# Kernel optimization log

Hardware: AMD Instinct MI355X
Metric: run time of the kernel (lower is better)

The kernel has to match this reference:

```python
import jax, jax.numpy as jnp
import numpy as np

LTH_THOLD = 0.0

def _mlp(x, w1, b1, w2, b2, w3, b3):
    # x: [b,h,s,d]; w*: [h,in,out]; per-head 3-layer MLP with SiLU
    h1 = jax.nn.silu(jnp.einsum('bhsd,hde->bhse', x, w1) + b1[None, :, None, :])
    h2 = jax.nn.silu(jnp.einsum('bhsd,hde->bhse', h1, w2) + b2[None, :, None, :])
    return jnp.einsum('bhsd,hde->bhse', h2, w3) + b3[None, :, None, :]

def setup_inputs() -> dict:
    key = jax.random.key(0)
    ks = jax.random.split(key, 16)
    b, h, s, d, idim, fdim = 2, 32, 2048, 128, 128, 32
    sc1 = 1.0 / np.sqrt(d); sc2 = 1.0 / np.sqrt(idim)
    def lin(k, fan_in, shape, sc):
        return jax.random.uniform(k, shape, jnp.float32, -sc, sc)
    inp = {
        'K': jax.random.normal(ks[0], (b, h, s, d), jnp.float32),
        'Q': jax.random.normal(ks[1], (b, h, s, d), jnp.float32),
        'wk1': lin(ks[2], d, (h, d, idim), sc1), 'bk1': lin(ks[3], d, (h, idim), sc1),
        'wk2': lin(ks[4], idim, (h, idim, idim), sc2), 'bk2': lin(ks[5], idim, (h, idim), sc2),
        'wk3': lin(ks[6], idim, (h, idim, fdim), sc2), 'bk3': lin(ks[7], idim, (h, fdim), sc2),
        'wq1': lin(ks[8], d, (h, d, idim), sc1), 'bq1': lin(ks[9], d, (h, idim), sc1),
        'wq2': lin(ks[10], idim, (h, idim, idim), sc2), 'bq2': lin(ks[11], idim, (h, idim), sc2),
        'wq3': lin(ks[12], idim, (h, idim, fdim), sc2), 'bq3': lin(ks[13], idim, (h, fdim), sc2),
    }
    return inp

def reference(K, Q, wk1, bk1, wk2, bk2, wk3, bk3, wq1, bq1, wq2, bq2, wq3, bq3):
    Klift = jnp.tanh(_mlp(K, wk1, bk1, wk2, bk2, wk3, bk3))  # [b,h,sk,32]
    Qlift = jnp.tanh(_mlp(Q, wq1, bq1, wq2, bq2, wq3, bq3))  # [b,h,sq,32]
    scores = jnp.einsum('bhtd,bhsd->bhts', Qlift, Klift)      # [b,h,sq,sk]
    sq, sk = Qlift.shape[2], Klift.shape[2]
    causal = jnp.tril(jnp.ones((sq, sk), bool), k=sk - sq)
    mask_value = jnp.finfo(scores.dtype).min
    scores = jnp.where(causal[None, None], scores, mask_value)
    scores = jax.nn.sigmoid(scores - LTH_THOLD)
    return (scores, Klift)
```

## Files before the change

kernel.cpp:

```cpp
#include <hip/hip_runtime.h>

typedef __attribute__((ext_vector_type(8))) short bf16x8;
typedef __attribute__((ext_vector_type(4))) float f32x4;

#define MFMA(a,b,c) __builtin_amdgcn_mfma_f32_16x16x32_bf16(a,b,c,0,0,0)

static __device__ __forceinline__ unsigned short f2bf(float f){
  unsigned u = __float_as_uint(f);
  u += 0x7FFF + ((u>>16)&1);
  return (unsigned short)(u>>16);
}
static __device__ __forceinline__ float bf2f(unsigned short b){
  return __uint_as_float(((unsigned)b)<<16);
}

__global__ __launch_bounds__(256) void wswz(
    const float* __restrict__ wk1, const float* __restrict__ wk2, const float* __restrict__ wk3,
    const float* __restrict__ wq1, const float* __restrict__ wq2, const float* __restrict__ wq3,
    unsigned short* __restrict__ wb)
{
  int y = blockIdx.y;
  int net = y / 3, layer = y % 3;
  const float* src = net ? (layer==0?wq1: layer==1?wq2:wq3)
                         : (layer==0?wk1: layer==1?wk2:wk3);
  int N  = (layer==2) ? 32 : 128;
  int NT = N / 16;
  int total = 32 * NT * 4 * 64;
  int e = blockIdx.x * 256 + threadIdx.x;
  if (e >= total) return;
  int lane = e & 63;
  int ks   = (e >> 6) & 3;
  int nt   = (e >> 8) % NT;
  int h    = (e >> 8) / NT;
  int k0 = ks*32 + 8*(lane>>4);
  int n0 = nt*16 + (lane&15);
  const float* s = src + (size_t)h*128*N + (size_t)k0*N + n0;
  unsigned short hi[8], lo[8];
  #pragma unroll
  for (int j=0;j<8;++j){
    float v = s[(size_t)j*N];
    unsigned short hh = f2bf(v);
    hi[j] = hh;
    lo[j] = f2bf(v - bf2f(hh));
  }
  size_t nb   = (size_t)net * 2359296;
  size_t loff = (layer==0) ? 0 : (layer==1) ? 1048576 : 2097152;
  size_t losz = (layer==2) ? 131072 : 524288;
  size_t eidx = ((((size_t)h*NT + nt)*4 + ks)*64 + lane)*8;
  unsigned short* dH = wb + nb + loff + eidx;
  unsigned short* dL = dH + losz;
  *(bf16x8*)dH = *(const bf16x8*)hi;
  *(bf16x8*)dL = *(const bf16x8*)lo;
}

__global__ __launch_bounds__(256,3) void lift(
    const float* __restrict__ Kin, const float* __restrict__ Qin,
    const float* __restrict__ bk1, const float* __restrict__ bk2, const float* __restrict__ bk3,
    const float* __restrict__ bq1, const float* __restrict__ bq2, const float* __restrict__ bq3,
    const unsigned short* __restrict__ wb,
    unsigned short* __restrict__ qlift, unsigned short* __restrict__ klift,
    float* __restrict__ kout)
{
  __shared__ unsigned short XH[64][136];
  __shared__ unsigned short XL[64][136];
  int bid = blockIdx.x;
  int h   = (bid & 7)*4 + ((bid>>3)&3);
  int st  = (bid>>5) & 31;
  int bb  = (bid>>10) & 1;
  int net = bid>>11;
  size_t rowbase = (size_t)(bb*32 + h)*2048 + (size_t)st*64;
  const float* X = (net ? Qin : Kin) + rowbase*128;
  const unsigned short* wn = wb + (size_t)net*2359296;
  const float* b1 = (net ? bq1 : bk1) + h*128;
  const float* b2 = (net ? bq2 : bk2) + h*128;
  const float* b3 = (net ? bq3 : bk3) + h*32;
  unsigned short* lifto = net ? qlift : klift;

  int tid = threadIdx.x, w = tid >> 6, l = tid & 63;
  int lr = l & 15, lg = l >> 4;
  int acol0 = 8*lg;

  #pragma unroll
  for (int i=0;i<8;++i){
    int row = i*8 + (tid>>5);
    int col = (tid&31)*4;
    float4 v = *(const float4*)&X[(size_t)row*128 + col];
    unsigned u0=__float_as_uint(v.x), u1=__float_as_uint(v.y),
             u2=__float_as_uint(v.z), u3=__float_as_uint(v.w);
    float l0 = v.x - __uint_as_float(u0 & 0xFFFF0000u);
    float l1 = v.y - __uint_as_float(u1 & 0xFFFF0000u);
    float l2 = v.z - __uint_as_float(u2 & 0xFFFF0000u);
    float l3 = v.w - __uint_as_float(u3 & 0xFFFF0000u);
    *(uint2*)&XH[row][col] = make_uint2((u0>>16) | (u1 & 0xFFFF0000u),
                                        (u2>>16) | (u3 & 0xFFFF0000u));
    *(uint2*)&XL[row][col] = make_uint2((__float_as_uint(l0)>>16) | (__float_as_uint(l1) & 0xFFFF0000u),
                                        (__float_as_uint(l2)>>16) | (__float_as_uint(l3) & 0xFFFF0000u));
  }
  __syncthreads();

  for (int L=0; L<2; ++L){
    const unsigned short* wH = wn + (size_t)L*1048576;
    const unsigned short* wL = wH + 524288;
    const float* bias = L ? b2 : b1;
    f32x4 acc[2][4];
    #pragma unroll
    for (int ntl=0;ntl<2;++ntl)
      #pragma unroll
      for (int rt=0;rt<4;++rt)
        acc[ntl][rt] = (f32x4){0.f,0.f,0.f,0.f};

    #pragma unroll
    for (int ks=0;ks<4;++ks){
      bf16x8 bh[2], bl[2];
      #pragma unroll
      for (int ntl=0;ntl<2;++ntl){
        size_t eidx = ((((size_t)h*8 + (w*2+ntl))*4 + ks)*64 + l)*8;
        bh[ntl] = *(const bf16x8*)(wH + eidx);
        bl[ntl] = *(const bf16x8*)(wL + eidx);
      }
      #pragma unroll
      for (int rt=0;rt<4;++rt){
        bf16x8 ah = *(const bf16x8*)&XH[rt*16+lr][ks*32 + acol0];
        bf16x8 al = *(const bf16x8*)&XL[rt*16+lr][ks*32 + acol0];
        #pragma unroll
        for (int ntl=0;ntl<2;++ntl){
          f32x4 a = acc[ntl][rt];
          a = MFMA(ah, bh[ntl], a);
          a = MFMA(al, bh[ntl], a);
          a = MFMA(ah, bl[ntl], a);
          acc[ntl][rt] = a;
        }
      }
    }
    __syncthreads();
    #pragma unroll
    for (int ntl=0;ntl<2;++ntl){
      int col = (w*2+ntl)*16 + lr;
      float bv = bias[col];
      #pragma unroll
      for (int rt=0;rt<4;++rt){
        #pragma unroll
        for (int i=0;i<4;++i){
          int row = rt*16 + 4*lg + i;
          float v = acc[ntl][rt][i] + bv;
          float sg = v * __builtin_amdgcn_rcpf(1.f + __expf(-v));
          unsigned u = __float_as_uint(sg);
          XH[row][col] = (unsigned short)(u>>16);
          float lo = sg - __uint_as_float(u & 0xFFFF0000u);
          XL[row][col] = (unsigned short)(__float_as_uint(lo)>>16);
        }
      }
    }
    __syncthreads();
  }

  {
    const unsigned short* wH = wn + 2097152;
    const unsigned short* wL = wH + 131072;
    int nt = w >> 1;
    int rb = (w & 1) * 2;
    f32x4 acc3[2];
    acc3[0] = (f32x4){0.f,0.f,0.f,0.f};
    acc3[1] = (f32x4){0.f,0.f,0.f,0.f};
    #pragma unroll
    for (int ks=0;ks<4;++ks){
      size_t eidx = ((((size_t)h*2 + nt)*4 + ks)*64 + l)*8;
      bf16x8 bh = *(const bf16x8*)(wH + eidx);
      bf16x8 bl = *(const bf16x8*)(wL + eidx);
      #pragma unroll
      for (int j=0;j<2;++j){
        bf16x8 ah = *(const bf16x8*)&XH[(rb+j)*16+lr][ks*32 + acol0];
        bf16x8 al = *(const bf16x8*)&XL[(rb+j)*16+lr][ks*32 + acol0];
        f32x4 a = acc3[j];
        a = MFMA(ah, bh, a);
        a = MFMA(al, bh, a);
        a = MFMA(ah, bl, a);
        acc3[j] = a;
      }
    }
    int col = nt*16 + lr;
    float bv = b3[col];
    #pragma unroll
    for (int j=0;j<2;++j){
      #pragma unroll
      for (int i=0;i<4;++i){
        int row = (rb+j)*16 + 4*lg + i;
        float v = acc3[j][i] + bv;
        float e2 = __expf(2.f*v);
        float t  = 1.f - 2.f*__builtin_amdgcn_rcpf(e2 + 1.f);
        size_t gro = (rowbase + (size_t)row)*32 + col;
        lifto[gro] = f2bf(t);
        if (net == 0) kout[gro] = t;
      }
    }
  }
}

__global__ __launch_bounds__(256) void scores_k(
    const unsigned short* __restrict__ qlift,
    const unsigned short* __restrict__ klift,
    float* __restrict__ out)
{
  int bid = blockIdx.x;
  int tc = bid & 15, tr = (bid >> 4) & 15, bh = bid >> 8;
  size_t sbase = (size_t)bh * 2048 * 2048;
  int r0 = tr * 128, c0 = tc * 128;
  int tid = threadIdx.x;

  if (tc > tr){
    float4 z = {0.f,0.f,0.f,0.f};
    #pragma unroll
    for (int it=0; it<16; ++it){
      int idx = it*256 + tid;
      int row = idx >> 5, c4 = idx & 31;
      *(float4*)&out[sbase + (size_t)(r0+row)*2048 + c0 + c4*4] = z;
    }
    return;
  }

  int w = tid >> 6, l = tid & 63;
  int lr = l & 15, lg = l >> 4;
  int acol0 = 8*lg;
  const unsigned short* qb = qlift + ((size_t)bh*2048 + r0 + w*32)*32;
  bf16x8 q0 = *(const bf16x8*)(qb + (size_t)lr*32 + acol0);
  bf16x8 q1 = *(const bf16x8*)(qb + (size_t)(16+lr)*32 + acol0);
  bool diag = (tc == tr);
  int t0 = r0 + w*32 + lr;
  int t1 = t0 + 16;

  const unsigned short* kb = klift + ((size_t)bh*2048 + c0)*32;
  bf16x8 kf[8];
  #pragma unroll
  for (int st8=0; st8<8; ++st8)
    kf[st8] = *(const bf16x8*)(kb + (size_t)(st8*16+lr)*32 + acol0);

  #pragma unroll
  for (int st8=0; st8<8; ++st8){
    f32x4 z4 = {0.f,0.f,0.f,0.f};
    f32x4 s0 = MFMA(kf[st8], q0, z4);
    f32x4 s1 = MFMA(kf[st8], q1, z4);
    int scol = c0 + st8*16 + 4*lg;
    f32x4 p0, p1;
    #pragma unroll
    for (int i=0;i<4;++i){
      float v0 = s0[i];
      float pv0 = __builtin_amdgcn_rcpf(1.f + __expf(-v0));
      if (diag && (scol + i > t0)) pv0 = 0.f;
      p0[i] = pv0;
      float v1 = s1[i];
      float pv1 = __builtin_amdgcn_rcpf(1.f + __expf(-v1));
      if (diag && (scol + i > t1)) pv1 = 0.f;
      p1[i] = pv1;
    }
    *(f32x4*)&out[sbase + (size_t)t0*2048 + scol] = p0;
    *(f32x4*)&out[sbase + (size_t)t1*2048 + scol] = p1;
  }
}

extern "C" void kernel_launch(void* const* d_in, const int* in_sizes, int n_in,
                              void* d_out, int out_size, void* d_ws, size_t ws_size,
                              hipStream_t stream) {
  const float* K   = (const float*)d_in[0];
  const float* Q   = (const float*)d_in[1];
  const float* wk1 = (const float*)d_in[2];  const float* bk1 = (const float*)d_in[3];
  const float* wk2 = (const float*)d_in[4];  const float* bk2 = (const float*)d_in[5];
  const float* wk3 = (const float*)d_in[6];  const float* bk3 = (const float*)d_in[7];
  const float* wq1 = (const float*)d_in[8];  const float* bq1 = (const float*)d_in[9];
  const float* wq2 = (const float*)d_in[10]; const float* bq2 = (const float*)d_in[11];
  const float* wq3 = (const float*)d_in[12]; const float* bq3 = (const float*)d_in[13];
  float* out = (float*)d_out;

  unsigned short* ws    = (unsigned short*)d_ws;
  unsigned short* qlift = ws;
  unsigned short* klift = ws + 4194304;
  unsigned short* wbase = ws + 8388608;

  hipLaunchKernelGGL(wswz, dim3(256,6), dim3(256), 0, stream,
                     wk1, wk2, wk3, wq1, wq2, wq3, wbase);
  hipLaunchKernelGGL(lift, dim3(4096), dim3(256), 0, stream,
                     K, Q, bk1, bk2, bk3, bq1, bq2, bq3,
                     wbase, qlift, klift, out + 268435456ull);
  hipLaunchKernelGGL(scores_k, dim3(16384), dim3(256), 0, stream,
                     qlift, klift, out);
}
```

Baseline: 319.5 us.

## Retile lift kernel to 32-row blocks with two waves each

The lift MLP kernel now processes 32 rows per block with 128 threads (2 waves), each wave covering 64 output columns across both row tiles, and the grid is doubled. This halves shared memory per block and gives more, smaller blocks, so occupancy and latency hiding may improve. In exchange each wave loads twice as many weight fragments per row computed, which raises global weight traffic per output, and the launch-bounds occupancy hint was dropped.

```diff
diff --git a/kernel.cpp b/kernel.cpp
--- a/kernel.cpp
+++ b/kernel.cpp
@@ -53,7 +53,7 @@
   *(bf16x8*)dL = *(const bf16x8*)lo;
 }
 
-__global__ __launch_bounds__(256,3) void lift(
+__global__ __launch_bounds__(128) void lift(
     const float* __restrict__ Kin, const float* __restrict__ Qin,
     const float* __restrict__ bk1, const float* __restrict__ bk2, const float* __restrict__ bk3,
     const float* __restrict__ bq1, const float* __restrict__ bq2, const float* __restrict__ bq3,
@@ -61,14 +61,15 @@
     unsigned short* __restrict__ qlift, unsigned short* __restrict__ klift,
     float* __restrict__ kout)
 {
-  __shared__ unsigned short XH[64][136];
-  __shared__ unsigned short XL[64][136];
+  __shared__ unsigned short XH[32][136];
+  __shared__ unsigned short XL[32][136];
   int bid = blockIdx.x;
-  int h   = (bid & 7)*4 + ((bid>>3)&3);
-  int st  = (bid>>5) & 31;
-  int bb  = (bid>>10) & 1;
-  int net = bid>>11;
-  size_t rowbase = (size_t)(bb*32 + h)*2048 + (size_t)st*64;
+  int h    = (bid & 7)*4 + ((bid>>3)&3);
+  int r    = bid >> 5;
+  int st32 = r & 63;
+  int bb   = (r>>6) & 1;
+  int net  = r>>7;
+  size_t rowbase = (size_t)(bb*32 + h)*2048 + (size_t)st32*32;
   const float* X = (net ? Qin : Kin) + rowbase*128;
   const unsigned short* wn = wb + (size_t)net*2359296;
   const float* b1 = (net ? bq1 : bk1) + h*128;
@@ -76,14 +77,15 @@
   const float* b3 = (net ? bq3 : bk3) + h*32;
   unsigned short* lifto = net ? qlift : klift;
 
-  int tid = threadIdx.x, w = tid >> 6, l = tid & 63;
+  int tid = threadIdx.x, wc = tid >> 6, l = tid & 63;
   int lr = l & 15, lg = l >> 4;
   int acol0 = 8*lg;
 
   #pragma unroll
   for (int i=0;i<8;++i){
-    int row = i*8 + (tid>>5);
-    int col = (tid&31)*4;
+    int idx = i*128 + tid;
+    int row = idx >> 5;
+    int col = (idx & 31)*4;
     float4 v = *(const float4*)&X[(size_t)row*128 + col];
     unsigned u0=__float_as_uint(v.x), u1=__float_as_uint(v.y),
              u2=__float_as_uint(v.z), u3=__float_as_uint(v.w);
@@ -102,28 +104,28 @@
     const unsigned short* wH = wn + (size_t)L*1048576;
     const unsigned short* wL = wH + 524288;
     const float* bias = L ? b2 : b1;
-    f32x4 acc[2][4];
-    #pragma unroll
-    for (int ntl=0;ntl<2;++ntl)
-      #pragma unroll
-      for (int rt=0;rt<4;++rt)
+    f32x4 acc[4][2];
+    #pragma unroll
+    for (int ntl=0;ntl<4;++ntl)
+      #pragma unroll
+      for (int rt=0;rt<2;++rt)
         acc[ntl][rt] = (f32x4){0.f,0.f,0.f,0.f};
 
     #pragma unroll
     for (int ks=0;ks<4;++ks){
-      bf16x8 bh[2], bl[2];
-      #pragma unroll
-      for (int ntl=0;ntl<2;++ntl){
-        size_t eidx = ((((size_t)h*8 + (w*2+ntl))*4 + ks)*64 + l)*8;
+      bf16x8 bh[4], bl[4];
+      #pragma unroll
+      for (int ntl=0;ntl<4;++ntl){
+        size_t eidx = ((((size_t)h*8 + (wc*4+ntl))*4 + ks)*64 + l)*8;
         bh[ntl] = *(const bf16x8*)(wH + eidx);
         bl[ntl] = *(const bf16x8*)(wL + eidx);
       }
       #pragma unroll
-      for (int rt=0;rt<4;++rt){
+      for (int rt=0;rt<2;++rt){
         bf16x8 ah = *(const bf16x8*)&XH[rt*16+lr][ks*32 + acol0];
         bf16x8 al = *(const bf16x8*)&XL[rt*16+lr][ks*32 + acol0];
         #pragma unroll
-        for (int ntl=0;ntl<2;++ntl){
+        for (int ntl=0;ntl<4;++ntl){
           f32x4 a = acc[ntl][rt];
           a = MFMA(ah, bh[ntl], a);
           a = MFMA(al, bh[ntl], a);
@@ -134,11 +136,11 @@
     }
     __syncthreads();
     #pragma unroll
-    for (int ntl=0;ntl<2;++ntl){
-      int col = (w*2+ntl)*16 + lr;
+    for (int ntl=0;ntl<4;++ntl){
+      int col = wc*64 + ntl*16 + lr;
       float bv = bias[col];
       #pragma unroll
-      for (int rt=0;rt<4;++rt){
+      for (int rt=0;rt<2;++rt){
         #pragma unroll
         for (int i=0;i<4;++i){
           int row = rt*16 + 4*lg + i;
@@ -157,35 +159,33 @@
   {
     const unsigned short* wH = wn + 2097152;
     const unsigned short* wL = wH + 131072;
-    int nt = w >> 1;
-    int rb = (w & 1) * 2;
     f32x4 acc3[2];
     acc3[0] = (f32x4){0.f,0.f,0.f,0.f};
     acc3[1] = (f32x4){0.f,0.f,0.f,0.f};
     #pragma unroll
     for (int ks=0;ks<4;++ks){
-      size_t eidx = ((((size_t)h*2 + nt)*4 + ks)*64 + l)*8;
+      size_t eidx = ((((size_t)h*2 + wc)*4 + ks)*64 + l)*8;
       bf16x8 bh = *(const bf16x8*)(wH + eidx);
       bf16x8 bl = *(const bf16x8*)(wL + eidx);
       #pragma unroll
-      for (int j=0;j<2;++j){
-        bf16x8 ah = *(const bf16x8*)&XH[(rb+j)*16+lr][ks*32 + acol0];
-        bf16x8 al = *(const bf16x8*)&XL[(rb+j)*16+lr][ks*32 + acol0];
-        f32x4 a = acc3[j];
+      for (int rt=0;rt<2;++rt){
+        bf16x8 ah = *(const bf16x8*)&XH[rt*16+lr][ks*32 + acol0];
+        bf16x8 al = *(const bf16x8*)&XL[rt*16+lr][ks*32 + acol0];
+        f32x4 a = acc3[rt];
         a = MFMA(ah, bh, a);
         a = MFMA(al, bh, a);
         a = MFMA(ah, bl, a);
-        acc3[j] = a;
-      }
-    }
-    int col = nt*16 + lr;
+        acc3[rt] = a;
+      }
+    }
+    int col = wc*16 + lr;
     float bv = b3[col];
     #pragma unroll
-    for (int j=0;j<2;++j){
+    for (int rt=0;rt<2;++rt){
       #pragma unroll
       for (int i=0;i<4;++i){
-        int row = (rb+j)*16 + 4*lg + i;
-        float v = acc3[j][i] + bv;
+        int row = rt*16 + 4*lg + i;
+        float v = acc3[rt][i] + bv;
         float e2 = __expf(2.f*v);
         float t  = 1.f - 2.f*__builtin_amdgcn_rcpf(e2 + 1.f);
         size_t gro = (rowbase + (size_t)row)*32 + col;
@@ -277,7 +277,7 @@
 
   hipLaunchKernelGGL(wswz, dim3(256,6), dim3(256), 0, stream,
                      wk1, wk2, wk3, wq1, wq2, wq3, wbase);
-  hipLaunchKernelGGL(lift, dim3(4096), dim3(256), 0, stream,
+  hipLaunchKernelGGL(lift, dim3(8192), dim3(128), 0, stream,
                      K, Q, bk1, bk2, bk3, bq1, bq2, bq3,
                      wbase, qlift, klift, out + 268435456ull);
   hipLaunchKernelGGL(scores_k, dim3(16384), dim3(256), 0, stream,
```

Measured after the change: 326.7 us. 2.3% more time.
